# Performance work log

Hardware: AMD Instinct MI355X
Metric: run time of the kernel (lower is better)

The kernel has to match this reference:

```python
import jax, jax.numpy as jnp
import numpy as np

N_HEAD = 16
ROPE_BASE = 10000.0

def _rotate_half(x):
    # matches torch: stack((-x[...,1::2], x[...,::2]), -1).flatten(-2)
    x1 = x[..., ::2]
    x2 = x[..., 1::2]
    return jnp.stack((-x2, x1), axis=-1).reshape(x.shape)

def setup_inputs() -> dict:
    key = jax.random.key(0)
    ks = jax.random.split(key, 5)
    B, T, C = 4, 2048, 1024
    x = jax.random.normal(ks[0], (B, T, C), dtype=jnp.float32)
    Wq = jax.random.normal(ks[1], (C, C), dtype=jnp.float32) * 0.02
    Wk = jax.random.normal(ks[2], (C, C), dtype=jnp.float32) * 0.02
    Wv = jax.random.normal(ks[3], (C, C), dtype=jnp.float32) * 0.02
    Wp = jax.random.normal(ks[4], (C, C), dtype=jnp.float32) * 0.02
    return {"x": x, "Wq": Wq, "Wk": Wk, "Wv": Wv, "Wp": Wp, "start_pos": 0}

def reference(x, Wq, Wk, Wv, Wp, start_pos):
    B, T, C = x.shape
    H = N_HEAD
    D = C // H
    # torch Linear: out = x @ W^T
    q = jnp.einsum('btc,dc->btd', x, Wq).reshape(B, T, H, D).transpose(0, 2, 1, 3)
    k = jnp.einsum('btc,dc->btd', x, Wk).reshape(B, T, H, D).transpose(0, 2, 1, 3)
    v = jnp.einsum('btc,dc->btd', x, Wv).reshape(B, T, H, D).transpose(0, 2, 1, 3)
    # RoPE cache (cat[freqs, freqs] with interleaved rotate_half, as in source)
    inv_freq = 1.0 / (ROPE_BASE ** (jnp.arange(0, D, 2, dtype=jnp.float32) / D))
    t = jnp.arange(T, dtype=jnp.float32) + jnp.float32(start_pos)
    freqs = t[:, None] * inv_freq[None, :]          # [T, D/2]
    emb = jnp.concatenate([freqs, freqs], axis=-1)  # [T, D]
    cos = jnp.cos(emb)[None, None]                  # [1,1,T,D]
    sin = jnp.sin(emb)[None, None]
    q = q * cos + _rotate_half(q) * sin
    k = k * cos + _rotate_half(k) * sin
    att = jnp.einsum('bhqd,bhkd->bhqk', q, k) / jnp.sqrt(jnp.float32(D))
    mask = jnp.triu(jnp.ones((T, T), dtype=bool), k=1)
    att = jnp.where(mask, -jnp.inf, att)
    att = jax.nn.softmax(att, axis=-1)
    y = jnp.einsum('bhqk,bhkd->bhqd', att, v)
    y = y.transpose(0, 2, 1, 3).reshape(B, T, C)
    return jnp.einsum('btc,dc->btd', y, Wp)
```

## Files before the change

### kernel.cpp

```cpp
#include <hip/hip_runtime.h>
#include <hip/hip_bf16.h>
#include <stdint.h>

#define B_  4
#define T_  2048
#define C_  1024
#define H_  16
#define D_  64
#define BT  (B_*T_)
#define KDIM 1024

typedef __attribute__((ext_vector_type(8))) short bf16x8;
typedef __attribute__((ext_vector_type(4))) float f32x4;

__device__ __forceinline__ unsigned short f2bf(float f) {
  union { float f; unsigned u; } v; v.f = f;
  unsigned r = v.u + 0x7FFFu + ((v.u >> 16) & 1u);
  return (unsigned short)(r >> 16);
}

__device__ __forceinline__ float exp2_fast(float x) {
  float r;
  asm("v_exp_f32 %0, %1" : "=v"(r) : "v"(x));
  return r;
}

__device__ __forceinline__ void gld_lds16(const void* g, void* l) {
  __builtin_amdgcn_global_load_lds(
      (__attribute__((address_space(1))) unsigned int*)(uintptr_t)g,
      (__attribute__((address_space(3))) unsigned int*)(unsigned)(uintptr_t)l,
      16, 0, 0);
}

__global__ __launch_bounds__(256) void k_convert(
    const float* __restrict__ x,  const float* __restrict__ wq,
    const float* __restrict__ wk, const float* __restrict__ wv,
    const float* __restrict__ wp,
    unsigned short* __restrict__ xb, unsigned short* __restrict__ wcat,
    unsigned short* __restrict__ wpb)
{
  const int NX = BT*C_/4;
  const int NW = C_*C_/4;
  const int TOT = NX + 4*NW;
  for (int i = blockIdx.x*blockDim.x + threadIdx.x; i < TOT; i += gridDim.x*blockDim.x) {
    const float4* src; unsigned short* dst; int idx;
    if (i < NX)                { src = (const float4*)x;  dst = xb;            idx = i; }
    else {
      int j = i - NX;
      if (j < NW)              { src = (const float4*)wq; dst = wcat;          idx = j; }
      else if (j < 2*NW)       { src = (const float4*)wk; dst = wcat + C_*C_;  idx = j - NW; }
      else if (j < 3*NW)       { src = (const float4*)wv; dst = wcat + 2*C_*C_;idx = j - 2*NW; }
      else                     { src = (const float4*)wp; dst = wpb;           idx = j - 3*NW; }
    }
    float4 v = src[idx];
    ushort4 o; o.x = f2bf(v.x); o.y = f2bf(v.y); o.z = f2bf(v.z); o.w = f2bf(v.w);
    *(ushort4*)(dst + (size_t)idx*4) = o;
  }
}

__global__ __launch_bounds__(256) void k_rope_tab(
    const int* __restrict__ start_pos, float* __restrict__ cosT, float* __restrict__ sinT)
{
  int i = blockIdx.x*blockDim.x + threadIdx.x;
  if (i >= T_*D_) return;
  int t = i >> 6, j = i & 63;
  float inv = exp2f(-(float)(j & 31) * (13.287712379549449f / 32.0f));
  float ang = (float)(t + start_pos[0]) * inv;
  cosT[i] = cosf(ang);
  sinT[i] = sinf(ang);
}

__global__ __launch_bounds__(512, 2) void k_gemm256(
    const unsigned short* __restrict__ A, const unsigned short* __restrict__ Bw,
    unsigned short* __restrict__ qb, unsigned short* __restrict__ kb,
    unsigned short* __restrict__ vt,
    const float* __restrict__ cosT, const float* __restrict__ sinT)
{
  __shared__ __attribute__((aligned(16))) char smem[131072];
  const int tid = threadIdx.x, l = tid & 63, w = tid >> 6;
  const int g = l >> 4, c = l & 15;
  const int m0 = blockIdx.x * 256, n0 = blockIdx.y * 256;
  const int wr = w >> 2, wc = w & 3;

  const char* srcA[4]; const char* srcB[4]; int dstP[4];
#pragma unroll
  for (int j = 0; j < 4; ++j) {
    int P = j*8192 + tid*16;
    int row = P >> 7;
    int Lb = P ^ ((row & 7) << 4);
    int col = (Lb & 127) >> 1;
    dstP[j] = P;
    srcA[j] = (const char*)A  + ((size_t)(m0 + row) * KDIM + col) * 2;
    srcB[j] = (const char*)Bw + ((size_t)(n0 + row) * KDIM + col) * 2;
  }

  f32x4 acc[8][4];
#pragma unroll
  for (int i = 0; i < 8; ++i)
#pragma unroll
    for (int j = 0; j < 4; ++j) acc[i][j] = (f32x4){0.f,0.f,0.f,0.f};

#pragma unroll
  for (int j = 0; j < 4; ++j) {
    gld_lds16(srcA[j], smem + dstP[j]);
    gld_lds16(srcB[j], smem + 32768 + dstP[j]);
  }

#define GPHASE(mb)                                                              \
  {                                                                             \
    bf16x8 af_[2][2];                                                           \
    _Pragma("unroll")                                                           \
    for (int m2 = 0; m2 < 2; ++m2)                                              \
      _Pragma("unroll")                                                         \
      for (int kk = 0; kk < 2; ++kk) {                                          \
        int row = wr*128 + ((mb) + m2)*16 + c;                                  \
        int Lb = row*128 + (kk*32 + g*8)*2;                                     \
        af_[m2][kk] = *(const bf16x8*)(smem + cur + (Lb ^ ((row & 7) << 4)));   \
      }                                                                         \
    __builtin_amdgcn_s_setprio(1);                                              \
    _Pragma("unroll")                                                           \
    for (int m2 = 0; m2 < 2; ++m2)                                              \
      _Pragma("unroll")                                                         \
      for (int ni = 0; ni < 4; ++ni)                                            \
        _Pragma("unroll")                                                       \
        for (int kk = 0; kk < 2; ++kk)                                          \
          acc[(mb)+m2][ni] = __builtin_amdgcn_mfma_f32_16x16x32_bf16(           \
              af_[m2][kk], bwf[ni][kk], acc[(mb)+m2][ni], 0, 0, 0);             \
    __builtin_amdgcn_s_setprio(0);                                              \
  }

  for (int t = 0; t < 16; ++t) {
    const int cur = (t & 1) << 16;
    const int nxt = cur ^ 65536;
    const int ko = (t + 1) * 128;

    asm volatile("s_waitcnt vmcnt(0)" ::: "memory");
    __builtin_amdgcn_s_barrier();

    if (t + 1 < 16) {
#pragma unroll
      for (int j = 0; j < 4; ++j)
        gld_lds16(srcA[j] + ko, smem + nxt + dstP[j]);
    }
    bf16x8 bwf[4][2];
#pragma unroll
    for (int ni = 0; ni < 4; ++ni)
#pragma unroll
      for (int kk = 0; kk < 2; ++kk) {
        int row = wc*64 + ni*16 + c;
        int Lb = row*128 + (kk*32 + g*8)*2;
        bwf[ni][kk] = *(const bf16x8*)(smem + (cur + 32768) + (Lb ^ ((row & 7) << 4)));
      }
    GPHASE(0)

    __builtin_amdgcn_s_barrier();
    if (t + 1 < 16) {
#pragma unroll
      for (int j = 0; j < 4; ++j)
        gld_lds16(srcB[j] + ko, smem + nxt + 32768 + dstP[j]);
    }
    GPHASE(2)

    __builtin_amdgcn_s_barrier();
    GPHASE(4)

    __builtin_amdgcn_s_barrier();
    GPHASE(6)
  }
#undef GPHASE

#pragma unroll
  for (int mi = 0; mi < 8; ++mi) {
#pragma unroll
    for (int ni = 0; ni < 4; ++ni) {
      const int mrow0 = m0 + wr*128 + mi*16 + g*4;
      const int ncol  = n0 + wc*64 + ni*16 + c;
      const int which = ncol >> 10;
      const int d = ncol & 1023, h = d >> 6, dd = d & 63;
      const int b = mrow0 >> 11, t0 = mrow0 & 2047;
      if (which == 2) {
        ushort4 o;
        o.x = f2bf(acc[mi][ni][0]); o.y = f2bf(acc[mi][ni][1]);
        o.z = f2bf(acc[mi][ni][2]); o.w = f2bf(acc[mi][ni][3]);
        *(ushort4*)(vt + ((size_t)((b*H_ + h)*D_ + dd))*T_ + t0) = o;
      } else {
#pragma unroll
        for (int r = 0; r < 4; ++r) {
          float val = acc[mi][ni][r];
          float partner = __shfl_xor(val, 1);
          float rot = (dd & 1) ? partner : -partner;
          float cv = cosT[(t0 + r)*64 + dd], sv = sinT[(t0 + r)*64 + dd];
          float o = val*cv + rot*sv;
          size_t oidx = (((size_t)(b*H_ + h))*T_ + (t0 + r))*D_ + dd;
          if (which == 0) qb[oidx] = f2bf(o * 0.180336879f);
          else            kb[oidx] = f2bf(o);
        }
      }
    }
  }
}

template<int EPI>
__global__ __launch_bounds__(256) void k_gemm(
    const unsigned short* __restrict__ A, const unsigned short* __restrict__ Bw,
    unsigned short* __restrict__ qb, unsigned short* __restrict__ kb,
    unsigned short* __restrict__ vt,
    const float* __restrict__ cosT, const float* __restrict__ sinT,
    float* __restrict__ outF)
{
  __shared__ __attribute__((aligned(16))) char smem[32768];
  const int tid = threadIdx.x, l = tid & 63, w = tid >> 6;
  const int g = l >> 4, c = l & 15;
  const int m0 = blockIdx.x * 128, n0 = blockIdx.y * 128;
  const int wr = w >> 1, wc = w & 1;

  const char* srcA[4]; const char* srcB[4]; int dstP[4];
#pragma unroll
  for (int j = 0; j < 4; ++j) {
    int P = w*4096 + j*1024 + l*16;
    int row = P >> 7;
    int Lb = P ^ ((row & 7) << 4);
    int col = (Lb & 127) >> 1;
    dstP[j] = P;
    srcA[j] = (const char*)A  + ((size_t)(m0 + row) * KDIM + col) * 2;
    srcB[j] = (const char*)Bw + ((size_t)(n0 + row) * KDIM + col) * 2;
  }

  f32x4 acc[4][4];
#pragma unroll
  for (int i = 0; i < 4; ++i)
#pragma unroll
    for (int j = 0; j < 4; ++j) acc[i][j] = (f32x4){0.f,0.f,0.f,0.f};

  for (int kt = 0; kt < KDIM; kt += 64) {
#pragma unroll
    for (int j = 0; j < 4; ++j) {
      gld_lds16(srcA[j] + kt*2, smem + dstP[j]);
      gld_lds16(srcB[j] + kt*2, smem + 16384 + dstP[j]);
    }
    __syncthreads();
#pragma unroll
    for (int kk = 0; kk < 2; ++kk) {
      bf16x8 af[4], bw4[4];
#pragma unroll
      for (int mi = 0; mi < 4; ++mi) {
        int row = wr*64 + mi*16 + c;
        int Lb = row*128 + (kk*32 + g*8)*2;
        af[mi] = *(const bf16x8*)(smem + (Lb ^ ((row & 7) << 4)));
      }
#pragma unroll
      for (int ni = 0; ni < 4; ++ni) {
        int row = wc*64 + ni*16 + c;
        int Lb = row*128 + (kk*32 + g*8)*2;
        bw4[ni] = *(const bf16x8*)(smem + 16384 + (Lb ^ ((row & 7) << 4)));
      }
#pragma unroll
      for (int mi = 0; mi < 4; ++mi)
#pragma unroll
        for (int ni = 0; ni < 4; ++ni)
          acc[mi][ni] = __builtin_amdgcn_mfma_f32_16x16x32_bf16(af[mi], bw4[ni], acc[mi][ni], 0, 0, 0);
    }
    __syncthreads();
  }

#pragma unroll
  for (int mi = 0; mi < 4; ++mi) {
#pragma unroll
    for (int ni = 0; ni < 4; ++ni) {
      const int mrow0 = m0 + wr*64 + mi*16 + g*4;
      const int ncol  = n0 + wc*64 + ni*16 + c;
      if (EPI == 1) {
#pragma unroll
        for (int r = 0; r < 4; ++r)
          outF[(size_t)(mrow0 + r) * 1024 + ncol] = acc[mi][ni][r];
      } else {
        const int which = ncol >> 10;
        const int d = ncol & 1023, h = d >> 6, dd = d & 63;
        const int b = mrow0 >> 11, t0 = mrow0 & 2047;
        if (which == 2) {
          ushort4 o;
          o.x = f2bf(acc[mi][ni][0]); o.y = f2bf(acc[mi][ni][1]);
          o.z = f2bf(acc[mi][ni][2]); o.w = f2bf(acc[mi][ni][3]);
          *(ushort4*)(vt + ((size_t)((b*H_ + h)*D_ + dd))*T_ + t0) = o;
        } else {
#pragma unroll
          for (int r = 0; r < 4; ++r) {
            float val = acc[mi][ni][r];
            float partner = __shfl_xor(val, 1);
            float rot = (dd & 1) ? partner : -partner;
            float cv = cosT[(t0 + r)*64 + dd], sv = sinT[(t0 + r)*64 + dd];
            float o = val*cv + rot*sv;
            size_t oidx = (((size_t)(b*H_ + h))*T_ + (t0 + r))*D_ + dd;
            if (which == 0) qb[oidx] = f2bf(o * 0.180336879f);
            else            kb[oidx] = f2bf(o);
          }
        }
      }
    }
  }
}

__global__ __launch_bounds__(256) void k_attn(
    const unsigned short* __restrict__ qb, const unsigned short* __restrict__ kb,
    const unsigned short* __restrict__ vt, unsigned short* __restrict__ yb)
{
  __shared__ __attribute__((aligned(16))) char smem[49152];
  const int tid = threadIdx.x, l = tid & 63, w = tid >> 6;
  const int g = l >> 4, c = l & 15;
  const int bh = blockIdx.y;
  const size_t bhO = (size_t)bh * T_ * D_;
  const int pbase = 32768 + w*4096;
  const int b = bh >> 4, h = bh & 15;

  const char* srcK[2]; const char* srcV[2]; int dstP2[2];
#pragma unroll
  for (int j = 0; j < 2; ++j) {
    int P = w*2048 + j*1024 + l*16;
    int row = P >> 7;
    int Lb = P ^ ((row & 7) << 4);
    int col = (Lb & 127) >> 1;
    dstP2[j] = P;
    srcK[j] = (const char*)(kb + bhO) + ((size_t)row*D_ + col)*2;
    srcV[j] = (const char*)(vt + bhO) + ((size_t)row*T_ + col)*2;
  }

  for (int half = 0; half < 2; ++half) {
    const int qt = half ? (int)blockIdx.x : (15 - (int)blockIdx.x);
    const int q0 = qt * 128;
    const int q0w = q0 + w*32;

    bf16x8 aq[2][2];
#pragma unroll
    for (int mi = 0; mi < 2; ++mi)
#pragma unroll
      for (int kc = 0; kc < 2; ++kc) {
        int row = q0w + mi*16 + c;
        aq[mi][kc] = *(const bf16x8*)(qb + bhO + (size_t)row*D_ + kc*32 + g*8);
      }

    f32x4 po[4][2];
    float mrun[2], lrun[2];
#pragma unroll
    for (int nd = 0; nd < 4; ++nd)
#pragma unroll
      for (int mi = 0; mi < 2; ++mi) po[nd][mi] = (f32x4){0.f,0.f,0.f,0.f};
    mrun[0] = mrun[1] = -1e30f; lrun[0] = lrun[1] = 0.f;

    const int nkt = (q0 + 128) >> 6;

#pragma unroll
    for (int j = 0; j < 2; ++j) {
      gld_lds16(srcK[j], smem + dstP2[j]);
      gld_lds16(srcV[j], smem + 8192 + dstP2[j]);
    }
    __syncthreads();

    for (int it = 0; it < nkt; ++it) {
      const int kv0 = it * 64;
      const int cur = (it & 1) * 16384;
      if (it + 1 < nkt) {
        const int nxt = 16384 - cur;
        const size_t ko = (size_t)(kv0 + 64) * 128;
        const size_t vo = (size_t)(kv0 + 64) * 2;
#pragma unroll
        for (int j = 0; j < 2; ++j) {
          gld_lds16(srcK[j] + ko, smem + nxt + dstP2[j]);
          gld_lds16(srcV[j] + vo, smem + nxt + 8192 + dstP2[j]);
        }
      }

      if (kv0 < q0w + 32) {
        f32x4 st[4][2];
#pragma unroll
        for (int ni = 0; ni < 4; ++ni)
#pragma unroll
          for (int mi = 0; mi < 2; ++mi) st[ni][mi] = (f32x4){0.f,0.f,0.f,0.f};
        __builtin_amdgcn_s_setprio(1);
#pragma unroll
        for (int kk = 0; kk < 2; ++kk) {
          bf16x8 bk[4];
#pragma unroll
          for (int ni = 0; ni < 4; ++ni) {
            int kn = ni*16 + c;
            int Lb = kn*128 + (kk*32 + g*8)*2;
            bk[ni] = *(const bf16x8*)(smem + cur + (Lb ^ ((kn & 7) << 4)));
          }
#pragma unroll
          for (int ni = 0; ni < 4; ++ni)
#pragma unroll
            for (int mi = 0; mi < 2; ++mi)
              st[ni][mi] = __builtin_amdgcn_mfma_f32_16x16x32_bf16(bk[ni], aq[mi][kk], st[ni][mi], 0, 0, 0);
        }
        __builtin_amdgcn_s_setprio(0);

        if (kv0 + 64 > q0w) {
#pragma unroll
          for (int ni = 0; ni < 4; ++ni)
#pragma unroll
            for (int r = 0; r < 4; ++r) {
              int kvv = kv0 + ni*16 + g*4 + r;
#pragma unroll
              for (int mi = 0; mi < 2; ++mi) {
                int qq = q0w + mi*16 + c;
                if (kvv > qq) st[ni][mi][r] = -1e30f;
              }
            }
        }

#pragma unroll
        for (int mi = 0; mi < 2; ++mi) {
          float mt = -1e30f;
#pragma unroll
          for (int ni = 0; ni < 4; ++ni)
#pragma unroll
            for (int r = 0; r < 4; ++r) mt = fmaxf(mt, st[ni][mi][r]);
          mt = fmaxf(mt, __shfl_xor(mt, 16));
          mt = fmaxf(mt, __shfl_xor(mt, 32));
          float m_use = mrun[mi];
          if (__any(mt > m_use + 8.f)) {
            float mnew = fmaxf(m_use, mt);
            float alpha = exp2_fast(m_use - mnew);
            mrun[mi] = mnew;
            m_use = mnew;
            lrun[mi] *= alpha;
#pragma unroll
            for (int nd = 0; nd < 4; ++nd)
#pragma unroll
              for (int r = 0; r < 4; ++r) po[nd][mi][r] *= alpha;
          }
          float rs = 0.f;
#pragma unroll
          for (int ni = 0; ni < 4; ++ni)
#pragma unroll
            for (int r = 0; r < 4; ++r) {
              float p = exp2_fast(st[ni][mi][r] - m_use);
              st[ni][mi][r] = p;
              rs += p;
            }
          lrun[mi] += rs;
        }

#pragma unroll
        for (int mi = 0; mi < 2; ++mi) {
          const int row = mi*16 + c;
          const int sw = (row & 7) << 4;
          const int rb = pbase + row*128;
#pragma unroll
          for (int ni = 0; ni < 4; ++ni) {
            unsigned u0, u1;
            asm("v_cvt_pk_bf16_f32 %0, %1, %2" : "=v"(u0) : "v"(st[ni][mi][0]), "v"(st[ni][mi][1]));
            asm("v_cvt_pk_bf16_f32 %0, %1, %2" : "=v"(u1) : "v"(st[ni][mi][2]), "v"(st[ni][mi][3]));
            int Lb = (ni*16 + g*4) * 2;
            uint2 uu; uu.x = u0; uu.y = u1;
            *(uint2*)(smem + rb + (Lb ^ sw)) = uu;
          }
        }

        __builtin_amdgcn_s_setprio(1);
#pragma unroll
        for (int kk = 0; kk < 2; ++kk) {
          bf16x8 pb[2];
#pragma unroll
          for (int mi = 0; mi < 2; ++mi) {
            int pr = mi*16 + c;
            int Lb = pr*128 + (kk*32 + g*8)*2;
            pb[mi] = *(const bf16x8*)(smem + pbase + (Lb ^ ((pr & 7) << 4)));
          }
          bf16x8 bv[4];
#pragma unroll
          for (int nd = 0; nd < 4; ++nd) {
            int vr = nd*16 + c;
            int Lb = vr*128 + (kk*32 + g*8)*2;
            bv[nd] = *(const bf16x8*)(smem + cur + 8192 + (Lb ^ ((vr & 7) << 4)));
          }
#pragma unroll
          for (int nd = 0; nd < 4; ++nd)
#pragma unroll
            for (int mi = 0; mi < 2; ++mi)
              po[nd][mi] = __builtin_amdgcn_mfma_f32_16x16x32_bf16(bv[nd], pb[mi], po[nd][mi], 0, 0, 0);
        }
        __builtin_amdgcn_s_setprio(0);
      }
      __syncthreads();
    }

#pragma unroll
    for (int mi = 0; mi < 2; ++mi) {
      float ls = lrun[mi];
      ls += __shfl_xor(ls, 16);
      ls += __shfl_xor(ls, 32);
      float inv = 1.f / ls;
      int t = q0w + mi*16 + c;
#pragma unroll
      for (int nd = 0; nd < 4; ++nd) {
        ushort4 o;
        o.x = f2bf(po[nd][mi][0] * inv);
        o.y = f2bf(po[nd][mi][1] * inv);
        o.z = f2bf(po[nd][mi][2] * inv);
        o.w = f2bf(po[nd][mi][3] * inv);
        *(ushort4*)(yb + ((size_t)b*T_ + t)*C_ + h*64 + nd*16 + g*4) = o;
      }
    }
  }
}

extern "C" void kernel_launch(void* const* d_in, const int* in_sizes, int n_in,
                              void* d_out, int out_size, void* d_ws, size_t ws_size,
                              hipStream_t stream)
{
  const float* x  = (const float*)d_in[0];
  const float* Wq = (const float*)d_in[1];
  const float* Wk = (const float*)d_in[2];
  const float* Wv = (const float*)d_in[3];
  const float* Wp = (const float*)d_in[4];
  const int*   sp = (const int*)d_in[5];
  float* out = (float*)d_out;

  char* ws = (char*)d_ws;
  unsigned short* xb   = (unsigned short*)(ws);
  unsigned short* wcat = (unsigned short*)(ws + 16777216);
  unsigned short* wpb  = (unsigned short*)(ws + 23068672);
  unsigned short* qb   = (unsigned short*)(ws + 25165824);
  unsigned short* kb   = (unsigned short*)(ws + 41943040);
  unsigned short* vt   = (unsigned short*)(ws + 58720256);
  unsigned short* yb   = (unsigned short*)(ws + 75497472);
  float* cosT = (float*)(ws + 92274688);
  float* sinT = (float*)(ws + 92798976);

  k_convert<<<dim3(2048), dim3(256), 0, stream>>>(x, Wq, Wk, Wv, Wp, xb, wcat, wpb);
  k_rope_tab<<<dim3(512), dim3(256), 0, stream>>>(sp, cosT, sinT);
  k_gemm256<<<dim3(32, 12), dim3(512), 0, stream>>>(xb, wcat, qb, kb, vt, cosT, sinT);
  k_attn<<<dim3(8, 64), dim3(256), 0, stream>>>(qb, kb, vt, yb);
  k_gemm<1><<<dim3(64, 8), dim3(256), 0, stream>>>(yb, wpb, nullptr, nullptr, nullptr, nullptr, nullptr, out);
}
```

Before: 181.0 us.

## Restructure QKV GEMM main loop into half-K stages with finer load pipelining

Rewrites the QKV projection GEMM's K loop. Each 128-wide K tile is split into two 64-wide halves with a new packed, swizzled LDS layout. Global-to-LDS loads are issued per half-stage and waited on with partial vmcnt counts, so only the needed data is awaited. Fragment reads become single 16-byte LDS loads per MFMA operand, fenced by sched_barrier, and the final iteration is peeled out. The goal is better overlap of memory traffic with MFMA work and fewer LDS reads, at the cost of more barriers and tighter, fragile waitcnt and ordering logic.

After: 184.6 us. About the same (+2.0%).

```diff
diff --git a/kernel.cpp b/kernel.cpp
--- a/kernel.cpp
+++ b/kernel.cpp
@@ -81,18 +81,25 @@
   const int g = l >> 4, c = l & 15;
   const int m0 = blockIdx.x * 256, n0 = blockIdx.y * 256;
   const int wr = w >> 2, wc = w & 3;
-
-  const char* srcA[4]; const char* srcB[4]; int dstP[4];
-#pragma unroll
-  for (int j = 0; j < 4; ++j) {
+  const char* gA = (const char*)A;
+  const char* gB = (const char*)Bw;
+
+  int dstU[2]; size_t aoff[2], boff[2];
+#pragma unroll
+  for (int j = 0; j < 2; ++j) {
     int P = j*8192 + tid*16;
-    int row = P >> 7;
-    int Lb = P ^ ((row & 7) << 4);
-    int col = (Lb & 127) >> 1;
-    dstP[j] = P;
-    srcA[j] = (const char*)A  + ((size_t)(m0 + row) * KDIM + col) * 2;
-    srcB[j] = (const char*)Bw + ((size_t)(n0 + row) * KDIM + col) * 2;
-  }
+    int p = P >> 7;
+    int inner = (P & 127) ^ ((p & 7) << 4);
+    int row = (p << 1) | (inner >> 6);
+    int kc = (inner & 63) >> 1;
+    dstU[j] = P;
+    aoff[j] = ((size_t)(m0 + row) * KDIM + kc) * 2;
+    boff[j] = ((size_t)(n0 + row) * KDIM + kc) * 2;
+  }
+
+  const int swzo = ((((c & 1) << 6) | (g << 4)) ^ (((c >> 1) & 7) << 4));
+  const int aB = (wr*64 + (c >> 1)) * 128 + swzo;
+  const int bB = 32768 + (wc*32 + (c >> 1)) * 128 + swzo;
 
   f32x4 acc[8][4];
 #pragma unroll
@@ -101,73 +108,107 @@
     for (int j = 0; j < 4; ++j) acc[i][j] = (f32x4){0.f,0.f,0.f,0.f};
 
 #pragma unroll
-  for (int j = 0; j < 4; ++j) {
-    gld_lds16(srcA[j], smem + dstP[j]);
-    gld_lds16(srcB[j], smem + 32768 + dstP[j]);
-  }
-
-#define GPHASE(mb)                                                              \
-  {                                                                             \
-    bf16x8 af_[2][2];                                                           \
-    _Pragma("unroll")                                                           \
-    for (int m2 = 0; m2 < 2; ++m2)                                              \
-      _Pragma("unroll")                                                         \
-      for (int kk = 0; kk < 2; ++kk) {                                          \
-        int row = wr*128 + ((mb) + m2)*16 + c;                                  \
-        int Lb = row*128 + (kk*32 + g*8)*2;                                     \
-        af_[m2][kk] = *(const bf16x8*)(smem + cur + (Lb ^ ((row & 7) << 4)));   \
-      }                                                                         \
-    __builtin_amdgcn_s_setprio(1);                                              \
-    _Pragma("unroll")                                                           \
-    for (int m2 = 0; m2 < 2; ++m2)                                              \
-      _Pragma("unroll")                                                         \
-      for (int ni = 0; ni < 4; ++ni)                                            \
-        _Pragma("unroll")                                                       \
-        for (int kk = 0; kk < 2; ++kk)                                          \
-          acc[(mb)+m2][ni] = __builtin_amdgcn_mfma_f32_16x16x32_bf16(           \
-              af_[m2][kk], bwf[ni][kk], acc[(mb)+m2][ni], 0, 0, 0);             \
-    __builtin_amdgcn_s_setprio(0);                                              \
-  }
-
-  for (int t = 0; t < 16; ++t) {
-    const int cur = (t & 1) << 16;
-    const int nxt = cur ^ 65536;
-    const int ko = (t + 1) * 128;
-
+  for (int j = 0; j < 2; ++j) gld_lds16(gA + aoff[j],      smem +     0 + dstU[j]);
+#pragma unroll
+  for (int j = 0; j < 2; ++j) gld_lds16(gB + boff[j],      smem + 32768 + dstU[j]);
+#pragma unroll
+  for (int j = 0; j < 2; ++j) gld_lds16(gA + aoff[j] + 64, smem + 16384 + dstU[j]);
+#pragma unroll
+  for (int j = 0; j < 2; ++j) gld_lds16(gB + boff[j] + 64, smem + 49152 + dstU[j]);
+  asm volatile("s_waitcnt vmcnt(4)" ::: "memory");
+  __builtin_amdgcn_s_barrier();
+
+#define MFMA16(MB)                                                               \
+    __builtin_amdgcn_s_setprio(1);                                               \
+    _Pragma("unroll")                                                            \
+    for (int i2 = 0; i2 < 4; ++i2)                                               \
+      _Pragma("unroll")                                                          \
+      for (int ni = 0; ni < 4; ++ni)                                             \
+        acc[(MB)+i2][ni] = __builtin_amdgcn_mfma_f32_16x16x32_bf16(              \
+            af[i2], bk[ni], acc[(MB)+i2][ni], 0, 0, 0);                          \
+    __builtin_amdgcn_s_setprio(0);
+
+#define PRE_MFMA                                                                 \
+    __builtin_amdgcn_s_barrier();                                                \
+    asm volatile("s_waitcnt lgkmcnt(0)" ::: "memory");                           \
+    __builtin_amdgcn_sched_barrier(0);
+
+  bf16x8 af[4], bk[4];
+
+#pragma unroll 2
+  for (int t = 0; t < 15; ++t) {
+    const int par = (t & 1) << 16;
+    const int nxt = par ^ 65536;
+    const size_t ko = (size_t)(t + 1) * 128;
+
+#pragma unroll
+    for (int i2 = 0; i2 < 4; ++i2) af[i2] = *(const bf16x8*)(smem + par + aB + i2*1024);
+#pragma unroll
+    for (int ni = 0; ni < 4; ++ni) bk[ni] = *(const bf16x8*)(smem + par + bB + ni*1024);
+#pragma unroll
+    for (int j = 0; j < 2; ++j) gld_lds16(gA + aoff[j] + ko, smem + nxt + dstU[j]);
+    PRE_MFMA
+    MFMA16(0)
+    __builtin_amdgcn_s_barrier();
+
+#pragma unroll
+    for (int i2 = 0; i2 < 4; ++i2) af[i2] = *(const bf16x8*)(smem + par + aB + (4+i2)*1024);
+#pragma unroll
+    for (int j = 0; j < 2; ++j) gld_lds16(gB + boff[j] + ko, smem + nxt + 32768 + dstU[j]);
+    PRE_MFMA
+    MFMA16(4)
+    asm volatile("s_waitcnt vmcnt(4)" ::: "memory");
+    __builtin_amdgcn_s_barrier();
+
+#pragma unroll
+    for (int i2 = 0; i2 < 4; ++i2) af[i2] = *(const bf16x8*)(smem + par + 16384 + aB + i2*1024);
+#pragma unroll
+    for (int ni = 0; ni < 4; ++ni) bk[ni] = *(const bf16x8*)(smem + par + 16384 + bB + ni*1024);
+#pragma unroll
+    for (int j = 0; j < 2; ++j) gld_lds16(gA + aoff[j] + ko + 64, smem + nxt + 16384 + dstU[j]);
+    PRE_MFMA
+    MFMA16(0)
+    __builtin_amdgcn_s_barrier();
+
+#pragma unroll
+    for (int i2 = 0; i2 < 4; ++i2) af[i2] = *(const bf16x8*)(smem + par + 16384 + aB + (4+i2)*1024);
+#pragma unroll
+    for (int j = 0; j < 2; ++j) gld_lds16(gB + boff[j] + ko + 64, smem + nxt + 49152 + dstU[j]);
+    PRE_MFMA
+    MFMA16(4)
+    asm volatile("s_waitcnt vmcnt(4)" ::: "memory");
+    __builtin_amdgcn_s_barrier();
+  }
+
+  {
+    const int par = 65536;
+#pragma unroll
+    for (int i2 = 0; i2 < 4; ++i2) af[i2] = *(const bf16x8*)(smem + par + aB + i2*1024);
+#pragma unroll
+    for (int ni = 0; ni < 4; ++ni) bk[ni] = *(const bf16x8*)(smem + par + bB + ni*1024);
+    PRE_MFMA
+    MFMA16(0)
+    __builtin_amdgcn_s_barrier();
+#pragma unroll
+    for (int i2 = 0; i2 < 4; ++i2) af[i2] = *(const bf16x8*)(smem + par + aB + (4+i2)*1024);
+    PRE_MFMA
+    MFMA16(4)
     asm volatile("s_waitcnt vmcnt(0)" ::: "memory");
     __builtin_amdgcn_s_barrier();
-
-    if (t + 1 < 16) {
-#pragma unroll
-      for (int j = 0; j < 4; ++j)
-        gld_lds16(srcA[j] + ko, smem + nxt + dstP[j]);
-    }
-    bf16x8 bwf[4][2];
-#pragma unroll
-    for (int ni = 0; ni < 4; ++ni)
-#pragma unroll
-      for (int kk = 0; kk < 2; ++kk) {
-        int row = wc*64 + ni*16 + c;
-        int Lb = row*128 + (kk*32 + g*8)*2;
-        bwf[ni][kk] = *(const bf16x8*)(smem + (cur + 32768) + (Lb ^ ((row & 7) << 4)));
-      }
-    GPHASE(0)
-
-    __builtin_amdgcn_s_barrier();
-    if (t + 1 < 16) {
-#pragma unroll
-      for (int j = 0; j < 4; ++j)
-        gld_lds16(srcB[j] + ko, smem + nxt + 32768 + dstP[j]);
-    }
-    GPHASE(2)
-
-    __builtin_amdgcn_s_barrier();
-    GPHASE(4)
-
-    __builtin_amdgcn_s_barrier();
-    GPHASE(6)
-  }
-#undef GPHASE
+#pragma unroll
+    for (int i2 = 0; i2 < 4; ++i2) af[i2] = *(const bf16x8*)(smem + par + 16384 + aB + i2*1024);
+#pragma unroll
+    for (int ni = 0; ni < 4; ++ni) bk[ni] = *(const bf16x8*)(smem + par + 16384 + bB + ni*1024);
+    PRE_MFMA
+    MFMA16(0)
+    __builtin_amdgcn_s_barrier();
+#pragma unroll
+    for (int i2 = 0; i2 < 4; ++i2) af[i2] = *(const bf16x8*)(smem + par + 16384 + aB + (4+i2)*1024);
+    PRE_MFMA
+    MFMA16(4)
+  }
+#undef MFMA16
+#undef PRE_MFMA
 
 #pragma unroll
   for (int mi = 0; mi < 8; ++mi) {
```
